# Performance work log

Hardware: AMD Instinct MI355X
Metric: run time of the kernel (lower is better)

## Reference

```python
import jax, jax.numpy as jnp
import numpy as np

N_LAYERS = 4
HIDDEN = 64
OUT_DIM = 32
IN_DIM = 32
NUM_GRAPHS = 128
N_NODES = 100000
N_EDGES = 1600000


def setup_inputs() -> dict:
    key = jax.random.key(0)
    ks = jax.random.split(key, 20)
    s = 0.05
    inp = {
        "x_q": jax.random.normal(ks[0], (N_NODES, IN_DIM), jnp.float32),
        "edge_index_q": jax.random.randint(ks[1], (2, N_EDGES), 0, N_NODES),
        "batch_q": jnp.sort(jax.random.randint(ks[2], (N_NODES,), 0, NUM_GRAPHS)),
        "x_c": jax.random.normal(ks[3], (N_NODES, IN_DIM), jnp.float32),
        "edge_index_c": jax.random.randint(ks[4], (2, N_EDGES), 0, N_NODES),
        "batch_c": jnp.sort(jax.random.randint(ks[5], (N_NODES,), 0, NUM_GRAPHS)),
        "pre_w": jax.random.normal(ks[6], (IN_DIM, HIDDEN), jnp.float32) * s,
        "pre_b": jnp.zeros((HIDDEN,), jnp.float32),
        "conv_w1": jax.random.normal(ks[7], (N_LAYERS, HIDDEN, HIDDEN), jnp.float32) * s,
        "conv_b1": jnp.zeros((N_LAYERS, HIDDEN), jnp.float32),
        "conv_w2": jax.random.normal(ks[8], (N_LAYERS, HIDDEN, HIDDEN), jnp.float32) * s,
        "conv_b2": jnp.zeros((N_LAYERS, HIDDEN), jnp.float32),
        "post_w1": jax.random.normal(ks[9], (HIDDEN * (N_LAYERS + 1), HIDDEN), jnp.float32) * s,
        "post_b1": jnp.zeros((HIDDEN,), jnp.float32),
        "post_w2": jax.random.normal(ks[10], (HIDDEN, OUT_DIM), jnp.float32) * s,
        "post_b2": jnp.zeros((OUT_DIM,), jnp.float32),
    }
    return inp


def _embed(x, edge_index, batch, pre_w, pre_b, conv_w1, conv_b1, conv_w2, conv_b2,
           post_w1, post_b1, post_w2, post_b2):
    n = x.shape[0]
    src, dst = edge_index[0], edge_index[1]
    x = x @ pre_w + pre_b                       # [N, H]
    emb = [x]
    xres = x
    for i in range(N_LAYERS):
        # GINConv (eps=0): nn(x + sum_{j in N(i)} x_j)
        agg = jax.ops.segment_sum(x[src], dst, num_segments=n)
        h = x + agg
        h = jax.nn.relu(h @ conv_w1[i] + conv_b1[i]) @ conv_w2[i] + conv_b2[i]
        if i & 1:
            h = h + xres
            xres = h
        x = jax.nn.relu(h)
        emb.append(x)
    e = jnp.concatenate(emb, axis=1)            # [N, H*(L+1)]
    g = jax.ops.segment_sum(e, batch, num_segments=NUM_GRAPHS)  # global_add_pool
    return jax.nn.relu(g @ post_w1 + post_b1) @ post_w2 + post_b2  # [G, OUT]


def reference(x_q, edge_index_q, batch_q, x_c, edge_index_c, batch_c,
              pre_w, pre_b, conv_w1, conv_b1, conv_w2, conv_b2,
              post_w1, post_b1, post_w2, post_b2):
    params = (pre_w, pre_b, conv_w1, conv_b1, conv_w2, conv_b2,
              post_w1, post_b1, post_w2, post_b2)
    gx = _embed(x_q, edge_index_q, batch_q, *params)
    hx = _embed(x_c, edge_index_c, batch_c, *params)
    # asymm_norm with all costs = 1: (del+edge_del)*0.5 = 1.0 each side
    return (jax.nn.relu(gx - hx) * 1.0).sum(-1) + (jax.nn.relu(hx - gx) * 1.0).sum(-1)
```

## Files before the change

kernel.cpp:

```cpp
#include <hip/hip_runtime.h>

#define NNODES 100000
#define NEDGES 1600000
#define NG 128
#define HID 64
#define INDIM 32
#define CAT 320
#define ODIM 32

#define BSH 6
#define NPB 64
#define NB ((NNODES + NPB - 1) / NPB)

#define SCAN_BLK 1024
#define NSCAN ((NNODES + SCAN_BLK - 1) / SCAN_BLK)

typedef unsigned short ushort_t;

__device__ __forceinline__ float bcast(float v, int lane) {
    return __uint_as_float(__builtin_amdgcn_readlane(__float_as_uint(v), lane));
}
__device__ __forceinline__ unsigned bcast_u(unsigned v, int lane) {
    return __builtin_amdgcn_readlane(v, lane);
}
__device__ __forceinline__ ushort_t f2bf(float f) {
    unsigned u = __float_as_uint(f);
    return (ushort_t)((u + 0x7FFFu + ((u >> 16) & 1u)) >> 16);
}
__device__ __forceinline__ float bf2f(ushort_t h) {
    return __uint_as_float(((unsigned)h) << 16);
}


__global__ void hist_kernel(const int* __restrict__ ei, int* __restrict__ counts) {
    int stride = gridDim.x * blockDim.x;
    for (int e = blockIdx.x * blockDim.x + threadIdx.x; e < NEDGES; e += stride)
        atomicAdd(&counts[ei[NEDGES + e]], 1);
}

__global__ void scan1_kernel(const int* __restrict__ counts, int* __restrict__ start,
                             int* __restrict__ bsums) {
    __shared__ int s[SCAN_BLK];
    int t = threadIdx.x;
    int i = blockIdx.x * SCAN_BLK + t;
    int v = (i < NNODES) ? counts[i] : 0;
    s[t] = v;
    for (int off = 1; off < SCAN_BLK; off <<= 1) {
        __syncthreads();
        int a = (t >= off) ? s[t - off] : 0;
        __syncthreads();
        s[t] += a;
    }
    __syncthreads();
    if (i < NNODES) start[i] = s[t] - v;
    if (t == SCAN_BLK - 1) bsums[blockIdx.x] = s[t];
}

__global__ void scan2_kernel(int* __restrict__ bsums) {
    __shared__ int s[128];
    int t = threadIdx.x;
    int v = (t < NSCAN) ? bsums[t] : 0;
    s[t] = v;
    for (int off = 1; off < 128; off <<= 1) {
        __syncthreads();
        int a = (t >= off) ? s[t - off] : 0;
        __syncthreads();
        s[t] += a;
    }
    __syncthreads();
    if (t < NSCAN) bsums[t] = s[t] - v;
}

__global__ void scan3_kernel(int* __restrict__ start, int* __restrict__ cursor,
                             const int* __restrict__ bsums) {
    int i = blockIdx.x * SCAN_BLK + threadIdx.x;
    if (i < NNODES) {
        int v = start[i] + bsums[blockIdx.x];
        start[i]  = v;
        cursor[i] = v;
    }
    if (i == 0) start[NNODES] = NEDGES;
}

__global__ void reorder_kernel(const int* __restrict__ ei, int* __restrict__ cursor,
                               unsigned* __restrict__ packed) {
    int stride = gridDim.x * blockDim.x;
    for (int e = blockIdx.x * blockDim.x + threadIdx.x; e < NEDGES; e += stride) {
        int dst = ei[NEDGES + e];
        int p = atomicAdd(&cursor[dst], 1);
        packed[p] = (unsigned)ei[e] | ((unsigned)(dst & (NPB - 1)) << 20);
    }
}


#define LOADV(vv, kk) { \
    const ushort_t* ap_ = Xb + (((size_t)(bcast_u(u, (kk)) & 0xFFFFFu)) << 6) + lane; \
    asm volatile("global_load_ushort %0, %1, off" : "=v"(vv) : "v"(ap_)); }

#define PROCJ(vv, kk, cnt) { \
    asm volatile("s_waitcnt vmcnt(" #cnt ")" ::: "memory"); \
    __builtin_amdgcn_sched_barrier(0); \
    int ld_ = (int)(bcast_u(u, (kk)) >> 20); \
    if (ld_ != cur) { \
        if (cur >= 0) atomicAdd(&tile[(cur << 6) + lane], acc); \
        acc = 0.f; cur = ld_; \
    } \
    acc += __uint_as_float((vv) << 16); }

#define LOAD8(P, base) \
    LOADV(P##0, (base)+0) LOADV(P##1, (base)+1) LOADV(P##2, (base)+2) LOADV(P##3, (base)+3) \
    LOADV(P##4, (base)+4) LOADV(P##5, (base)+5) LOADV(P##6, (base)+6) LOADV(P##7, (base)+7)

#define PROC8_HI(P, base) \
    PROCJ(P##0,(base)+0,15) PROCJ(P##1,(base)+1,14) PROCJ(P##2,(base)+2,13) PROCJ(P##3,(base)+3,12) \
    PROCJ(P##4,(base)+4,11) PROCJ(P##5,(base)+5,10) PROCJ(P##6,(base)+6,9)  PROCJ(P##7,(base)+7,8)

#define PROC8_LO(P, base) \
    PROCJ(P##0,(base)+0,7) PROCJ(P##1,(base)+1,6) PROCJ(P##2,(base)+2,5) PROCJ(P##3,(base)+3,4) \
    PROCJ(P##4,(base)+4,3) PROCJ(P##5,(base)+5,2) PROCJ(P##6,(base)+6,1) PROCJ(P##7,(base)+7,0)

__global__ void __launch_bounds__(256, 5) fused_kernel(
        const ushort_t* __restrict__ Xb, ushort_t* __restrict__ Xb_out,
        float* __restrict__ XRES, float* __restrict__ G,
        const int* __restrict__ batch,
        const unsigned* __restrict__ packed, const int* __restrict__ start,
        const float* __restrict__ w1, const float* __restrict__ b1,
        const float* __restrict__ w2, const float* __restrict__ b2,
        int do_res, int stage) {
    __shared__ float tile[NPB * HID];
    __shared__ float sw[HID * HID];
    int blk = blockIdx.x;
    for (int i = threadIdx.x; i < NPB * HID; i += blockDim.x) tile[i] = 0.f;
    {
        const float4* w4 = (const float4*)w1;
        float4* s4 = (float4*)sw;
        for (int i = threadIdx.x; i < HID * HID / 4; i += blockDim.x) s4[i] = w4[i];
    }
    __syncthreads();
    int lane   = threadIdx.x & 63;
    int wave   = threadIdx.x >> 6;
    int nw     = blockDim.x >> 6;
    int node0  = blk << BSH;
    int nvalid = min(NPB, NNODES - node0);
    int eb = start[node0];
    int ee = start[node0 + nvalid];
    for (int base = eb + wave * 64; base < ee; base += nw * 64) {
        int nv = min(64, ee - base);
        unsigned u = (base + lane < ee) ? packed[base + lane] : 0u;
        float acc = 0.f;
        int   cur = -1;
        if (nv == 64) {
            unsigned p0,p1,p2,p3,p4,p5,p6,p7, q0,q1,q2,q3,q4,q5,q6,q7;
            LOAD8(p, 0)
            LOAD8(q, 8)
            PROC8_HI(p, 0)
            LOAD8(p, 16)
            PROC8_HI(q, 8)
            LOAD8(q, 24)
            PROC8_HI(p, 16)
            LOAD8(p, 32)
            PROC8_HI(q, 24)
            LOAD8(q, 40)
            PROC8_HI(p, 32)
            LOAD8(p, 48)
            PROC8_HI(q, 40)
            LOAD8(q, 56)
            PROC8_HI(p, 48)
            PROC8_LO(q, 56)
        } else {
            for (int k = 0; k < nv; ++k) {
                unsigned uj = bcast_u(u, k);
                float vv = bf2f(Xb[((size_t)(uj & 0xFFFFFu) << 6) + lane]);
                atomicAdd(&tile[((uj >> 20) << 6) + lane], vv);
            }
        }
        if (cur >= 0) atomicAdd(&tile[(cur << 6) + lane], acc);
    }
    __syncthreads();
    int per = NPB >> 2;
    int n0w = node0 + wave * per;
    int n1w = min(n0w + per, node0 + nvalid);
    if (n0w < n1w) {
        float bb1 = b1[lane];
        for (int node = n0w; node < n1w; ++node) {
            int row = (node - node0) << 6;
            float in   = bf2f(Xb[((size_t)node << 6) + lane]) + tile[row + lane];
            float acc1 = bb1;
#pragma unroll
            for (int k = 0; k < HID; ++k)
                acc1 = fmaf(bcast(in, k), sw[k * HID + lane], acc1);
            tile[row + lane] = fmaxf(acc1, 0.f);
        }
    }
    __syncthreads();
    {
        const float4* w4 = (const float4*)w2;
        float4* s4 = (float4*)sw;
        for (int i = threadIdx.x; i < HID * HID / 4; i += blockDim.x) s4[i] = w4[i];
    }
    __syncthreads();
    if (n0w < n1w) {
        float bb2 = b2[lane];
        float pool = 0.f;
        int   curg = batch[n0w];
        for (int node = n0w; node < n1w; ++node) {
            float acc2 = bb2;
            const float4* trow = (const float4*)&tile[(node - node0) << 6];
#pragma unroll
            for (int k4 = 0; k4 < HID / 4; ++k4) {
                float4 h = trow[k4];
                acc2 = fmaf(h.x, sw[(4 * k4 + 0) * HID + lane], acc2);
                acc2 = fmaf(h.y, sw[(4 * k4 + 1) * HID + lane], acc2);
                acc2 = fmaf(h.z, sw[(4 * k4 + 2) * HID + lane], acc2);
                acc2 = fmaf(h.w, sw[(4 * k4 + 3) * HID + lane], acc2);
            }
            if (do_res) {
                acc2 += XRES[((size_t)node << 6) + lane];
                XRES[((size_t)node << 6) + lane] = acc2;
            }
            float xn = fmaxf(acc2, 0.f);
            Xb_out[((size_t)node << 6) + lane] = f2bf(xn);
            int g = batch[node];
            if (g != curg) {
                atomicAdd(&G[curg * CAT + stage * HID + lane], pool);
                pool = 0.f; curg = g;
            }
            pool += xn;
        }
        atomicAdd(&G[curg * CAT + stage * HID + lane], pool);
    }
}


__global__ void pre_kernel(const float* __restrict__ xin, const int* __restrict__ batch,
                           const float* __restrict__ w, const float* __restrict__ b,
                           ushort_t* __restrict__ Xb, float* __restrict__ XRES,
                           float* __restrict__ G) {
    __shared__ float sw[INDIM * HID];
    for (int i = threadIdx.x; i < INDIM * HID; i += blockDim.x) sw[i] = w[i];
    __syncthreads();
    int lane = threadIdx.x & 63;
    int wid  = blockIdx.x * (blockDim.x >> 6) + (threadIdx.x >> 6);
    int nW   = gridDim.x * (blockDim.x >> 6);
    int chunk = (NNODES + nW - 1) / nW;
    int n0 = wid * chunk, n1 = min(n0 + chunk, NNODES);
    if (n0 >= n1) return;
    float bb   = b[lane];
    float pool = 0.f;
    int   curg = batch[n0];
    for (int node = n0; node < n1; ++node) {
        float in  = (lane < INDIM) ? xin[node * INDIM + lane] : 0.f;
        float acc = bb;
#pragma unroll
        for (int k = 0; k < INDIM; ++k)
            acc = fmaf(bcast(in, k), sw[k * HID + lane], acc);
        Xb[((size_t)node << 6) + lane]   = f2bf(acc);
        XRES[((size_t)node << 6) + lane] = acc;
        int g = batch[node];
        if (g != curg) {
            atomicAdd(&G[curg * CAT + lane], pool);
            pool = 0.f; curg = g;
        }
        pool += acc;
    }
    atomicAdd(&G[curg * CAT + lane], pool);
}

__global__ void post_kernel(const float* __restrict__ GQ, const float* __restrict__ GC,
                            const float* __restrict__ w1, const float* __restrict__ b1,
                            const float* __restrict__ w2, const float* __restrict__ b2,
                            float* __restrict__ out) {
    int g    = blockIdx.x;
    int lane = threadIdx.x;
    __shared__ float h1q[HID], h1c[HID];
    float aq = b1[lane], ac = b1[lane];
    for (int k = 0; k < CAT; ++k) {
        float w = w1[k * HID + lane];
        aq = fmaf(GQ[g * CAT + k], w, aq);
        ac = fmaf(GC[g * CAT + k], w, ac);
    }
    h1q[lane] = fmaxf(aq, 0.f);
    h1c[lane] = fmaxf(ac, 0.f);
    __syncthreads();
    float s = 0.f;
    if (lane < ODIM) {
        float oq = b2[lane], oc = b2[lane];
        for (int k = 0; k < HID; ++k) {
            float w = w2[k * ODIM + lane];
            oq = fmaf(h1q[k], w, oq);
            oc = fmaf(h1c[k], w, oc);
        }
        s = fabsf(oq - oc);
    }
    for (int off = 16; off; off >>= 1) s += __shfl_down(s, off, 64);
    if (lane == 0) out[g] = s;
}

extern "C" void kernel_launch(void* const* d_in, const int* in_sizes, int n_in,
                              void* d_out, int out_size, void* d_ws, size_t ws_size,
                              hipStream_t stream) {
    const float* x_q     = (const float*)d_in[0];
    const int*   ei_q    = (const int*)d_in[1];
    const int*   batch_q = (const int*)d_in[2];
    const float* x_c     = (const float*)d_in[3];
    const int*   ei_c    = (const int*)d_in[4];
    const int*   batch_c = (const int*)d_in[5];
    const float* pre_w   = (const float*)d_in[6];
    const float* pre_b   = (const float*)d_in[7];
    const float* conv_w1 = (const float*)d_in[8];
    const float* conv_b1 = (const float*)d_in[9];
    const float* conv_w2 = (const float*)d_in[10];
    const float* conv_b2 = (const float*)d_in[11];
    const float* post_w1 = (const float*)d_in[12];
    const float* post_b1 = (const float*)d_in[13];
    const float* post_w2 = (const float*)d_in[14];
    const float* post_b2 = (const float*)d_in[15];

    float* ws   = (float*)d_ws;
    float* XRES = ws;
    float* GQ   = XRES + NNODES * HID;
    float* GC   = GQ + NG * CAT;
    int*   counts = (int*)(GC + NG * CAT);
    int*   start  = counts + NNODES;
    int*   cursor = start + NNODES + 1;
    unsigned* packed = (unsigned*)(cursor + NNODES);
    int*   bsums  = (int*)(packed + NEDGES);
    ushort_t* XbfA = (ushort_t*)(bsums + NSCAN + 2);
    ushort_t* XbfB = XbfA + (size_t)NNODES * HID;

    hipMemsetAsync(GQ, 0, 2 * NG * CAT * sizeof(float), stream);

    for (int side = 0; side < 2; ++side) {
        const float* xin   = side ? x_c : x_q;
        const int*   ei    = side ? ei_c : ei_q;
        const int*   batch = side ? batch_c : batch_q;
        float*       G     = side ? GC : GQ;

        hipMemsetAsync(counts, 0, NNODES * sizeof(int), stream);
        hist_kernel<<<2048, 256, 0, stream>>>(ei, counts);
        scan1_kernel<<<NSCAN, SCAN_BLK, 0, stream>>>(counts, start, bsums);
        scan2_kernel<<<1, 128, 0, stream>>>(bsums);
        scan3_kernel<<<NSCAN, SCAN_BLK, 0, stream>>>(start, cursor, bsums);
        reorder_kernel<<<2048, 256, 0, stream>>>(ei, cursor, packed);

        pre_kernel<<<1024, 256, 0, stream>>>(xin, batch, pre_w, pre_b, XbfA, XRES, G);

        ushort_t* xcur = XbfA;
        ushort_t* xnxt = XbfB;
        for (int l = 0; l < 4; ++l) {
            fused_kernel<<<NB, 256, 0, stream>>>(xcur, xnxt, XRES, G, batch, packed, start,
                                                 conv_w1 + l * HID * HID, conv_b1 + l * HID,
                                                 conv_w2 + l * HID * HID, conv_b2 + l * HID,
                                                 l & 1, l + 1);
            ushort_t* t = xcur; xcur = xnxt; xnxt = t;
        }
    }

    post_kernel<<<NG, 64, 0, stream>>>(GQ, GC, post_w1, post_b1, post_w2, post_b2,
                                       (float*)d_out);
}
```

Baseline: 1.541 ms.

## Replace atomic counting-sort CSR build with two-pass LDS radix sort

Builds the destination-sorted edge list with a two-level radix sort instead of the old per-node global histogram, multi-kernel scan and atomic scatter. Edges are first bucketed into 512-node coarse buckets using LDS histograms and block-local staging. Each bucket is then sorted by fine destination in shared memory, which also writes the CSR start offsets. This avoids heavily contended global atomics and random global writes, at the cost of an extra pass over the edges and a fallback path when a bucket exceeds LDS capacity.

```diff
diff --git a/kernel.cpp b/kernel.cpp
--- a/kernel.cpp
+++ b/kernel.cpp
@@ -12,8 +12,11 @@
 #define NPB 64
 #define NB ((NNODES + NPB - 1) / NPB)
 
-#define SCAN_BLK 1024
-#define NSCAN ((NNODES + SCAN_BLK - 1) / SCAN_BLK)
+#define CBSH 9
+#define NCB ((NNODES + 511) / 512)
+#define R1CHUNK 4096
+#define NR1 ((NEDGES + R1CHUNK - 1) / R1CHUNK)
+#define CAP 12288
 
 typedef unsigned short ushort_t;
 
@@ -32,63 +35,125 @@
 }
 
 
-__global__ void hist_kernel(const int* __restrict__ ei, int* __restrict__ counts) {
+__global__ void radix1a_kernel(const int* __restrict__ ei, int* __restrict__ ccounts) {
+    __shared__ int h[NCB];
+    for (int i = threadIdx.x; i < NCB; i += blockDim.x) h[i] = 0;
+    __syncthreads();
     int stride = gridDim.x * blockDim.x;
     for (int e = blockIdx.x * blockDim.x + threadIdx.x; e < NEDGES; e += stride)
-        atomicAdd(&counts[ei[NEDGES + e]], 1);
-}
-
-__global__ void scan1_kernel(const int* __restrict__ counts, int* __restrict__ start,
-                             int* __restrict__ bsums) {
-    __shared__ int s[SCAN_BLK];
+        atomicAdd(&h[ei[NEDGES + e] >> CBSH], 1);
+    __syncthreads();
+    for (int i = threadIdx.x; i < NCB; i += blockDim.x)
+        if (h[i]) atomicAdd(&ccounts[i], h[i]);
+}
+
+__global__ void cscan_kernel(const int* __restrict__ ccounts, int* __restrict__ cstart,
+                             int* __restrict__ ccursor) {
+    __shared__ int s[256];
     int t = threadIdx.x;
-    int i = blockIdx.x * SCAN_BLK + t;
-    int v = (i < NNODES) ? counts[i] : 0;
+    int v = (t < NCB) ? ccounts[t] : 0;
     s[t] = v;
-    for (int off = 1; off < SCAN_BLK; off <<= 1) {
+    for (int off = 1; off < 256; off <<= 1) {
         __syncthreads();
         int a = (t >= off) ? s[t - off] : 0;
         __syncthreads();
         s[t] += a;
     }
     __syncthreads();
-    if (i < NNODES) start[i] = s[t] - v;
-    if (t == SCAN_BLK - 1) bsums[blockIdx.x] = s[t];
-}
-
-__global__ void scan2_kernel(int* __restrict__ bsums) {
-    __shared__ int s[128];
+    if (t < NCB) { cstart[t] = s[t] - v; ccursor[t] = s[t] - v; }
+    if (t == 0) cstart[NCB] = NEDGES;
+}
+
+__global__ void __launch_bounds__(256) radix1b_kernel(
+        const int* __restrict__ ei, int* __restrict__ ccursor,
+        unsigned* __restrict__ packed0) {
+    __shared__ int h[256], lstart[256], lpos[256], gbase[256], sc[256];
+    __shared__ unsigned sdata[R1CHUNK];
+    int t  = threadIdx.x;
+    int e0 = blockIdx.x * R1CHUNK;
+    int e1 = min(e0 + R1CHUNK, NEDGES);
+    h[t] = 0; lpos[t] = 0;
+    __syncthreads();
+    for (int e = e0 + t; e < e1; e += blockDim.x)
+        atomicAdd(&h[ei[NEDGES + e] >> CBSH], 1);
+    __syncthreads();
+    int v = h[t];
+    sc[t] = v;
+    for (int off = 1; off < 256; off <<= 1) {
+        __syncthreads();
+        int a = (t >= off) ? sc[t - off] : 0;
+        __syncthreads();
+        sc[t] += a;
+    }
+    __syncthreads();
+    lstart[t] = sc[t] - v;
+    if (t < NCB && v) gbase[t] = atomicAdd(&ccursor[t], v);
+    __syncthreads();
+    for (int e = e0 + t; e < e1; e += blockDim.x) {
+        int dst = ei[NEDGES + e];
+        int b   = dst >> CBSH;
+        int p   = lstart[b] + atomicAdd(&lpos[b], 1);
+        sdata[p] = (unsigned)ei[e] | ((unsigned)(dst & 511) << 20);
+    }
+    __syncthreads();
+    int lane = t & 63, wave = t >> 6;
+    for (int b = wave; b < NCB; b += 4) {
+        int cnt = h[b];
+        if (!cnt) continue;
+        int gb = gbase[b], ls = lstart[b];
+        for (int i = lane; i < cnt; i += 64) packed0[gb + i] = sdata[ls + i];
+    }
+}
+
+__global__ void __launch_bounds__(256) radix2_kernel(
+        const unsigned* __restrict__ packed0, const int* __restrict__ cstart,
+        int* __restrict__ start, unsigned* __restrict__ packed) {
+    __shared__ int cnt[512], excl[512], lpos[512], sc[256];
+    __shared__ unsigned sdata[CAP];
+    int b = blockIdx.x;
     int t = threadIdx.x;
-    int v = (t < NSCAN) ? bsums[t] : 0;
-    s[t] = v;
-    for (int off = 1; off < 128; off <<= 1) {
-        __syncthreads();
-        int a = (t >= off) ? s[t - off] : 0;
-        __syncthreads();
-        s[t] += a;
-    }
-    __syncthreads();
-    if (t < NSCAN) bsums[t] = s[t] - v;
-}
-
-__global__ void scan3_kernel(int* __restrict__ start, int* __restrict__ cursor,
-                             const int* __restrict__ bsums) {
-    int i = blockIdx.x * SCAN_BLK + threadIdx.x;
-    if (i < NNODES) {
-        int v = start[i] + bsums[blockIdx.x];
-        start[i]  = v;
-        cursor[i] = v;
-    }
-    if (i == 0) start[NNODES] = NEDGES;
-}
-
-__global__ void reorder_kernel(const int* __restrict__ ei, int* __restrict__ cursor,
-                               unsigned* __restrict__ packed) {
-    int stride = gridDim.x * blockDim.x;
-    for (int e = blockIdx.x * blockDim.x + threadIdx.x; e < NEDGES; e += stride) {
-        int dst = ei[NEDGES + e];
-        int p = atomicAdd(&cursor[dst], 1);
-        packed[p] = (unsigned)ei[e] | ((unsigned)(dst & (NPB - 1)) << 20);
+    int s0 = cstart[b], s1 = cstart[b + 1];
+    int n  = s1 - s0;
+    for (int i = t; i < 512; i += 256) { cnt[i] = 0; lpos[i] = 0; }
+    __syncthreads();
+    for (int i = t; i < n; i += 256)
+        atomicAdd(&cnt[(packed0[s0 + i] >> 20) & 511], 1);
+    __syncthreads();
+    int a  = cnt[2 * t], c2 = cnt[2 * t + 1];
+    int ps = a + c2;
+    sc[t] = ps;
+    for (int off = 1; off < 256; off <<= 1) {
+        __syncthreads();
+        int x = (t >= off) ? sc[t - off] : 0;
+        __syncthreads();
+        sc[t] += x;
+    }
+    __syncthreads();
+    int ex = sc[t] - ps;
+    excl[2 * t] = ex; excl[2 * t + 1] = ex + a;
+    __syncthreads();
+    int node0 = b << CBSH;
+    for (int j = t; j < 512; j += 256) {
+        int node = node0 + j;
+        if (node < NNODES) start[node] = s0 + excl[j];
+    }
+    if (b == 0 && t == 0) start[NNODES] = NEDGES;
+    if (n <= CAP) {
+        for (int i = t; i < n; i += 256) {
+            unsigned u = packed0[s0 + i];
+            int ld = (u >> 20) & 511;
+            int p  = excl[ld] + atomicAdd(&lpos[ld], 1);
+            sdata[p] = (u & 0xFFFFFu) | ((unsigned)(ld & 63) << 20);
+        }
+        __syncthreads();
+        for (int i = t; i < n; i += 256) packed[s0 + i] = sdata[i];
+    } else {
+        for (int i = t; i < n; i += 256) {
+            unsigned u = packed0[s0 + i];
+            int ld = (u >> 20) & 511;
+            int p  = s0 + excl[ld] + atomicAdd(&lpos[ld], 1);
+            packed[p] = (u & 0xFFFFFu) | ((unsigned)(ld & 63) << 20);
+        }
     }
 }
 
@@ -320,12 +385,13 @@
     float* XRES = ws;
     float* GQ   = XRES + NNODES * HID;
     float* GC   = GQ + NG * CAT;
-    int*   counts = (int*)(GC + NG * CAT);
-    int*   start  = counts + NNODES;
-    int*   cursor = start + NNODES + 1;
-    unsigned* packed = (unsigned*)(cursor + NNODES);
-    int*   bsums  = (int*)(packed + NEDGES);
-    ushort_t* XbfA = (ushort_t*)(bsums + NSCAN + 2);
+    int*   ccounts = (int*)(GC + NG * CAT);
+    int*   cstart  = ccounts + NCB;
+    int*   ccursor = cstart + NCB + 1;
+    int*   start   = ccursor + NCB;
+    unsigned* packed0 = (unsigned*)(start + NNODES + 1);
+    unsigned* packed  = packed0 + NEDGES;
+    ushort_t* XbfA = (ushort_t*)(packed + NEDGES);
     ushort_t* XbfB = XbfA + (size_t)NNODES * HID;
 
     hipMemsetAsync(GQ, 0, 2 * NG * CAT * sizeof(float), stream);
@@ -336,12 +402,11 @@
         const int*   batch = side ? batch_c : batch_q;
         float*       G     = side ? GC : GQ;
 
-        hipMemsetAsync(counts, 0, NNODES * sizeof(int), stream);
-        hist_kernel<<<2048, 256, 0, stream>>>(ei, counts);
-        scan1_kernel<<<NSCAN, SCAN_BLK, 0, stream>>>(counts, start, bsums);
-        scan2_kernel<<<1, 128, 0, stream>>>(bsums);
-        scan3_kernel<<<NSCAN, SCAN_BLK, 0, stream>>>(start, cursor, bsums);
-        reorder_kernel<<<2048, 256, 0, stream>>>(ei, cursor, packed);
+        hipMemsetAsync(ccounts, 0, NCB * sizeof(int), stream);
+        radix1a_kernel<<<256, 256, 0, stream>>>(ei, ccounts);
+        cscan_kernel<<<1, 256, 0, stream>>>(ccounts, cstart, ccursor);
+        radix1b_kernel<<<NR1, 256, 0, stream>>>(ei, ccursor, packed0);
+        radix2_kernel<<<NCB, 256, 0, stream>>>(packed0, cstart, start, packed);
 
         pre_kernel<<<1024, 256, 0, stream>>>(xin, batch, pre_w, pre_b, XbfA, XRES, G);
 
```

New measurement: 1.254 ms. 1.23x faster.
